# Kernel optimization log

Measured on AMD Instinct MI355X. Metric: run time of the kernel, lower is better.

## Reference

```python
import jax, jax.numpy as jnp
import numpy as np

CTX = 1024   # context_window
D = 512      # emb_dim
B = 8        # batch


def make_rotary_matrix(ctx, d):
    """Dense block-diagonal RoPE rotation matrices R: [ctx, d, d]."""
    pos = jnp.arange(ctx, dtype=jnp.float32)[:, None]          # [ctx, 1]
    i = jnp.arange(d // 2, dtype=jnp.float32)                  # [d/2]
    theta = pos / (10000.0 ** (2.0 * i / d))                   # [ctx, d/2]
    cos, sin = jnp.cos(theta), jnp.sin(theta)
    idx = jnp.arange(d // 2)
    R = jnp.zeros((ctx, d, d), jnp.float32)
    R = R.at[:, 2 * idx, 2 * idx].set(cos)
    R = R.at[:, 2 * idx, 2 * idx + 1].set(-sin)
    R = R.at[:, 2 * idx + 1, 2 * idx].set(sin)
    R = R.at[:, 2 * idx + 1, 2 * idx + 1].set(cos)
    return R


def setup_inputs() -> dict:
    key = jax.random.key(0)
    ks = jax.random.split(key, 8)
    s = 1.0 / np.sqrt(D)
    inp = {
        "x": jax.random.normal(ks[0], (B, CTX, D), jnp.float32),
        "w_q": jax.random.uniform(ks[1], (D, D), jnp.float32, -s, s),
        "b_q": jax.random.uniform(ks[2], (D,), jnp.float32, -s, s),
        "w_k": jax.random.uniform(ks[3], (D, D), jnp.float32, -s, s),
        "b_k": jax.random.uniform(ks[4], (D,), jnp.float32, -s, s),
        "w_v": jax.random.uniform(ks[5], (D, D), jnp.float32, -s, s),
        "b_v": jax.random.uniform(ks[6], (D,), jnp.float32, -s, s),
        "R": make_rotary_matrix(CTX, D),
        "kv_cache": 0,  # bool flag; does not affect output
    }
    return inp


def reference(x, w_q, b_q, w_k, b_k, w_v, b_v, R, kv_cache):
    B_, C, Dm = x.shape
    q = x @ w_q.T + b_q                      # [B, C, D]
    k = x @ w_k.T + b_k
    v = x @ w_v.T + b_v
    Rc = R[:C]                               # [C, D, D]
    # torch.bmm(q.transpose(0,1), R.transpose(1,2)).transpose(0,1)
    # out[b,c,e] = sum_d q[b,c,d] * R[c,e,d]
    q_rot = jnp.einsum("bcd,ced->bce", q, Rc)
    k_rot = jnp.einsum("bcd,ced->bce", k, Rc)
    # causal SDPA (eval mode: dropout omitted)
    scale = 1.0 / jnp.sqrt(jnp.asarray(Dm, jnp.float32))
    scores = jnp.einsum("bqe,bke->bqk", q_rot, k_rot) * scale   # [B, C, C]
    causal = jnp.tril(jnp.ones((C, C), bool))
    scores = jnp.where(causal, scores, jnp.finfo(scores.dtype).min)
    attn = jax.nn.softmax(scores, axis=-1)
    return jnp.einsum("bqk,bkd->bqd", attn, v)
```

## Files before the change

### kernel.cpp

```cpp
#include <hip/hip_runtime.h>

#define BATCH 8
#define CTXN  1024
#define DMODEL 512

using short8  = __attribute__((ext_vector_type(8))) short;
using f32x16  = __attribute__((ext_vector_type(16))) float;

typedef const void __attribute__((address_space(1)))* as1_cvp;
typedef void __attribute__((address_space(3)))* as3_vp;

__device__ __forceinline__ unsigned short f2bf(float f) {
  unsigned int u = __float_as_uint(f);
  u += 0x7fffu + ((u >> 16) & 1u);
  return (unsigned short)(u >> 16);
}
__device__ __forceinline__ float bf2f(unsigned short u) {
  return __uint_as_float((unsigned int)u << 16);
}

#define X4  1048576
#define W4  65536
#define CAST_BLOCKS 4864
__global__ __launch_bounds__(256) void prep_all(const float* __restrict__ x,
                                                const float* __restrict__ wq,
                                                const float* __restrict__ wk,
                                                const float* __restrict__ wv,
                                                unsigned short* __restrict__ xb,
                                                unsigned short* __restrict__ wb,
                                                float2* __restrict__ tab) {
  if (blockIdx.x < CAST_BLOCKS) {
    int gid = blockIdx.x * 256 + threadIdx.x;
    const float4* src; ushort4* dst;
    if (gid < X4)                { src = (const float4*)x  + gid;              dst = (ushort4*)xb + gid; }
    else if (gid < X4 + W4)      { int o = gid - X4;        src = (const float4*)wq + o; dst = (ushort4*)wb + o; }
    else if (gid < X4 + 2 * W4)  { int o = gid - X4 - W4;   src = (const float4*)wk + o; dst = (ushort4*)(wb + 262144) + o; }
    else                         { int o = gid - X4 - 2*W4; src = (const float4*)wv + o; dst = (ushort4*)(wb + 524288) + o; }
    float4 f = *src;
    ushort4 u;
    u.x = f2bf(f.x); u.y = f2bf(f.y); u.z = f2bf(f.z); u.w = f2bf(f.w);
    *dst = u;
  } else {
    int c = blockIdx.x - CAST_BLOCKS;
    int i = threadIdx.x;
    float freq = exp2f((float)i * (-13.287712379549449f / 256.0f));
    float th = (float)c * freq;
    float sn, cs;
    sincosf(th, &sn, &cs);
    tab[c * 256 + i] = make_float2(cs, sn);
  }
}

__device__ __forceinline__ void issue_tile(const unsigned short* __restrict__ gA, int ldA,
                                           const unsigned short* __restrict__ gB, int ldB,
                                           unsigned short* sA, unsigned short* sB,
                                           int slot, int tid) {
  unsigned short* dA = sA + (slot << 13);
  unsigned short* dB = sB + (slot << 13);
#pragma unroll
  for (int c = 0; c < 2; ++c) {
    int li  = (c << 9) + tid;
    int row = li >> 3;
    int ch  = (li & 7) ^ (row & 7);
    __builtin_amdgcn_global_load_lds((as1_cvp)(gA + (size_t)row * ldA + (ch << 3)),
                                     (as3_vp)(dA + (li << 3)), 16, 0, 0);
  }
#pragma unroll
  for (int c = 0; c < 2; ++c) {
    int li  = (c << 9) + tid;
    int row = li >> 3;
    int ch  = (li & 7) ^ (row & 7);
    __builtin_amdgcn_global_load_lds((as1_cvp)(gB + (size_t)row * ldB + (ch << 3)),
                                     (as3_vp)(dB + (li << 3)), 16, 0, 0);
  }
}

__device__ __forceinline__ void gemm_pipe(const unsigned short* __restrict__ gA, int ldA,
                                          const unsigned short* __restrict__ gB, int ldB,
                                          int nt, unsigned short* sA, unsigned short* sB,
                                          int tid, f32x16 acc[2]) {
  const int l = tid & 63, w = tid >> 6, wr = w >> 2, wc = w & 3;
  const int cl = l & 31, hi = l >> 5;
  int aoff[2][4], boff[4];
#pragma unroll
  for (int m = 0; m < 2; ++m) {
    int ra = wr * 64 + m * 32 + cl;
#pragma unroll
    for (int ks = 0; ks < 4; ++ks) {
      int kc = ks * 2 + hi;
      aoff[m][ks] = ra * 64 + ((kc ^ (ra & 7)) << 3);
    }
  }
  {
    int rb = wc * 32 + cl;
#pragma unroll
    for (int ks = 0; ks < 4; ++ks) {
      int kc = ks * 2 + hi;
      boff[ks] = rb * 64 + ((kc ^ (rb & 7)) << 3);
    }
  }
  issue_tile(gA, ldA, gB, ldB, sA, sB, 0, tid);
  issue_tile(gA + 64, ldA, gB + 64, ldB, sA, sB, 1, tid);
  asm volatile("s_waitcnt vmcnt(4)" ::: "memory");
  __builtin_amdgcn_s_barrier();
  __builtin_amdgcn_sched_barrier(0);

  for (int t = 0; t < nt; ++t) {
    const unsigned short* sAb = sA + ((t & 1) << 13);
    const unsigned short* sBb = sB + ((t & 1) << 13);
    short8 af[2][4], bfv[4];
    af[0][0] = *(const short8*)(sAb + aoff[0][0]);
    af[1][0] = *(const short8*)(sAb + aoff[1][0]);
    bfv[0]   = *(const short8*)(sBb + boff[0]);
#pragma unroll
    for (int ks = 0; ks < 3; ++ks) {
      af[0][ks + 1] = *(const short8*)(sAb + aoff[0][ks + 1]);
      af[1][ks + 1] = *(const short8*)(sAb + aoff[1][ks + 1]);
      bfv[ks + 1]   = *(const short8*)(sBb + boff[ks + 1]);
      asm volatile("s_waitcnt lgkmcnt(3)" ::: "memory");
      __builtin_amdgcn_sched_barrier(0);
      __builtin_amdgcn_s_setprio(1);
      acc[0] = __builtin_amdgcn_mfma_f32_32x32x16_bf16(af[0][ks], bfv[ks], acc[0], 0, 0, 0);
      acc[1] = __builtin_amdgcn_mfma_f32_32x32x16_bf16(af[1][ks], bfv[ks], acc[1], 0, 0, 0);
      __builtin_amdgcn_s_setprio(0);
    }
    asm volatile("s_waitcnt lgkmcnt(0)" ::: "memory");
    __builtin_amdgcn_sched_barrier(0);
    __builtin_amdgcn_s_barrier();
    if (t + 2 < nt) {
      issue_tile(gA + (size_t)(t + 2) * 64, ldA, gB + (size_t)(t + 2) * 64, ldB, sA, sB, t & 1, tid);
      asm volatile("s_waitcnt vmcnt(4)" ::: "memory");
    } else {
      asm volatile("s_waitcnt vmcnt(0)" ::: "memory");
    }
    __builtin_amdgcn_sched_barrier(0);
    __builtin_amdgcn_s_setprio(1);
    acc[0] = __builtin_amdgcn_mfma_f32_32x32x16_bf16(af[0][3], bfv[3], acc[0], 0, 0, 0);
    acc[1] = __builtin_amdgcn_mfma_f32_32x32x16_bf16(af[1][3], bfv[3], acc[1], 0, 0, 0);
    __builtin_amdgcn_s_setprio(0);
    __builtin_amdgcn_s_barrier();
    __builtin_amdgcn_sched_barrier(0);
  }
}

__device__ __forceinline__ void issue_tile64(const unsigned short* __restrict__ gA, int ldA,
                                             const unsigned short* __restrict__ gB, int ldB,
                                             unsigned short* sA, unsigned short* sB,
                                             int slot, int tid) {
  unsigned short* dA = sA + (slot << 12);
  unsigned short* dB = sB + (slot << 13);
#pragma unroll
  for (int c = 0; c < 2; ++c) {
    int li  = (c << 8) + tid;
    int row = li >> 3;
    int ch  = (li & 7) ^ (row & 7);
    __builtin_amdgcn_global_load_lds((as1_cvp)(gA + (size_t)row * ldA + (ch << 3)),
                                     (as3_vp)(dA + (li << 3)), 16, 0, 0);
  }
#pragma unroll
  for (int c = 0; c < 4; ++c) {
    int li  = (c << 8) + tid;
    int row = li >> 3;
    int ch  = (li & 7) ^ (row & 7);
    __builtin_amdgcn_global_load_lds((as1_cvp)(gB + (size_t)row * ldB + (ch << 3)),
                                     (as3_vp)(dB + (li << 3)), 16, 0, 0);
  }
}

template <bool RSUM>
__device__ __forceinline__ void gemm_pipe64(const unsigned short* __restrict__ gA, int ldA,
                                            const unsigned short* __restrict__ gB, int ldB,
                                            int nt, unsigned short* sA, unsigned short* sB,
                                            int tid, f32x16 acc[2], float* lacc) {
  const int l = tid & 63, w = tid >> 6;
  const int cl = l & 31, hi = l >> 5;
  int aoff[2][4], boff[4];
#pragma unroll
  for (int m = 0; m < 2; ++m) {
    int ra = m * 32 + cl;
#pragma unroll
    for (int ks = 0; ks < 4; ++ks) {
      int kc = ks * 2 + hi;
      aoff[m][ks] = ra * 64 + ((kc ^ (ra & 7)) << 3);
    }
  }
  {
    int rb = w * 32 + cl;
#pragma unroll
    for (int ks = 0; ks < 4; ++ks) {
      int kc = ks * 2 + hi;
      boff[ks] = rb * 64 + ((kc ^ (rb & 7)) << 3);
    }
  }
  const int srow = tid >> 2;
  const int kc0  = (tid & 3) * 2;
  const int soff0 = srow * 64 + (((kc0)     ^ (srow & 7)) << 3);
  const int soff1 = srow * 64 + (((kc0 + 1) ^ (srow & 7)) << 3);

  issue_tile64(gA, ldA, gB, ldB, sA, sB, 0, tid);
  issue_tile64(gA + 64, ldA, gB + 64, ldB, sA, sB, 1, tid);
  asm volatile("s_waitcnt vmcnt(6)" ::: "memory");
  __builtin_amdgcn_s_barrier();
  __builtin_amdgcn_sched_barrier(0);

  for (int t = 0; t < nt; ++t) {
    const unsigned short* sAb = sA + ((t & 1) << 12);
    const unsigned short* sBb = sB + ((t & 1) << 13);
    short8 af[2][4], bfv[4], sr0, sr1;
    af[0][0] = *(const short8*)(sAb + aoff[0][0]);
    af[1][0] = *(const short8*)(sAb + aoff[1][0]);
    bfv[0]   = *(const short8*)(sBb + boff[0]);
#pragma unroll
    for (int ks = 0; ks < 3; ++ks) {
      af[0][ks + 1] = *(const short8*)(sAb + aoff[0][ks + 1]);
      af[1][ks + 1] = *(const short8*)(sAb + aoff[1][ks + 1]);
      bfv[ks + 1]   = *(const short8*)(sBb + boff[ks + 1]);
      asm volatile("s_waitcnt lgkmcnt(3)" ::: "memory");
      __builtin_amdgcn_sched_barrier(0);
      __builtin_amdgcn_s_setprio(1);
      acc[0] = __builtin_amdgcn_mfma_f32_32x32x16_bf16(af[0][ks], bfv[ks], acc[0], 0, 0, 0);
      acc[1] = __builtin_amdgcn_mfma_f32_32x32x16_bf16(af[1][ks], bfv[ks], acc[1], 0, 0, 0);
      __builtin_amdgcn_s_setprio(0);
    }
    if (RSUM) {
      sr0 = *(const short8*)(sAb + soff0);
      sr1 = *(const short8*)(sAb + soff1);
    }
    asm volatile("s_waitcnt lgkmcnt(0)" ::: "memory");
    __builtin_amdgcn_sched_barrier(0);
    __builtin_amdgcn_s_barrier();
    if (t + 2 < nt) {
      issue_tile64(gA + (size_t)(t + 2) * 64, ldA, gB + (size_t)(t + 2) * 64, ldB, sA, sB, t & 1, tid);
      asm volatile("s_waitcnt vmcnt(6)" ::: "memory");
    } else {
      asm volatile("s_waitcnt vmcnt(0)" ::: "memory");
    }
    __builtin_amdgcn_sched_barrier(0);
    if (RSUM) {
      float ls = 0.0f;
#pragma unroll
      for (int j = 0; j < 8; ++j) ls += bf2f((unsigned short)sr0[j]) + bf2f((unsigned short)sr1[j]);
      *lacc += ls;
    }
    __builtin_amdgcn_s_setprio(1);
    acc[0] = __builtin_amdgcn_mfma_f32_32x32x16_bf16(af[0][3], bfv[3], acc[0], 0, 0, 0);
    acc[1] = __builtin_amdgcn_mfma_f32_32x32x16_bf16(af[1][3], bfv[3], acc[1], 0, 0, 0);
    __builtin_amdgcn_s_setprio(0);
    __builtin_amdgcn_s_barrier();
    __builtin_amdgcn_sched_barrier(0);
  }
}


__global__ __launch_bounds__(512, 4) void qkv_kernel(const unsigned short* __restrict__ xb,
                                                     const unsigned short* __restrict__ wb,
                                                     const float* __restrict__ bq,
                                                     const float* __restrict__ bk,
                                                     const float* __restrict__ bv,
                                                     const float2* __restrict__ tab,
                                                     unsigned short* __restrict__ qrot,
                                                     unsigned short* __restrict__ krot,
                                                     unsigned short* __restrict__ vt) {
  __shared__ __align__(16) unsigned short sA[2 * 8192];
  __shared__ __align__(16) unsigned short sB[2 * 8192];
  int id = blockIdx.x;
  int b3 = id & 7, rest = id >> 3;
  int ntile = rest % 12, mhi = rest / 12;
  int m0 = (mhi * 8 + b3) * 128, n0 = ntile * 128;
  int t = threadIdx.x, w = t >> 6, l = t & 63, wr = w >> 2, wc = w & 3;
  int cl = l & 31, hi = l >> 5;
  f32x16 acc[2] = {};
  gemm_pipe(xb + (size_t)m0 * 512, 512, wb + (size_t)n0 * 512, 512, 8, sA, sB, t, acc);

  int sec = n0 >> 9;
  const float* bias = (sec == 0) ? bq : (sec == 1) ? bk : bv;
  unsigned short* qk_dst = (sec == 0) ? qrot : krot;
  int e = (n0 + wc * 32 + cl) & 511;
  float bsv = bias[e];
  if (sec < 2) {
    int i2 = e >> 1;
#pragma unroll
    for (int m = 0; m < 2; ++m) {
      int rowb = m0 + wr * 64 + m * 32 + 4 * hi;
#pragma unroll
      for (int r = 0; r < 16; ++r) {
        int mg = rowb + (r & 3) + 8 * (r >> 2);
        int cpos = mg & (CTXN - 1);
        float val  = acc[m][r] + bsv;
        float part = __shfl_xor(val, 1);
        float2 cs  = tab[cpos * 256 + i2];
        float o = (e & 1) ? fmaf(part, cs.y, val * cs.x)
                          : fmaf(-part, cs.y, val * cs.x);
        qk_dst[(size_t)mg * 512 + e] = f2bf(o);
      }
    }
  } else {
#pragma unroll
    for (int m = 0; m < 2; ++m) {
      int rowb0 = m0 + wr * 64 + m * 32 + 4 * hi;
#pragma unroll
      for (int q = 0; q < 4; ++q) {
        int rowb = rowb0 + 8 * q;
        int bidx = rowb >> 10;
        int cpos = rowb & (CTXN - 1);
        ushort4 pk;
        pk.x = f2bf(acc[m][q * 4 + 0] + bsv);
        pk.y = f2bf(acc[m][q * 4 + 1] + bsv);
        pk.z = f2bf(acc[m][q * 4 + 2] + bsv);
        pk.w = f2bf(acc[m][q * 4 + 3] + bsv);
        *(ushort4*)(vt + ((size_t)bidx * 512 + e) * 1024 + cpos) = pk;
      }
    }
  }
}

__device__ const unsigned char T64_IT[72] = {
  0,1,2,2,3,3,4,4,4,5,5,5,6,6,6,6,7,7,7,7,
  8,8,8,8,8,9,9,9,9,9,10,10,10,10,10,10,11,11,11,11,11,11,
  12,12,12,12,12,12,12,13,13,13,13,13,13,13,
  14,14,14,14,14,14,14,14,15,15,15,15,15,15,15,15};
__device__ const unsigned char T64_JT[72] = {
  0,0,0,1,0,1,0,1,2,0,1,2,0,1,2,3,0,1,2,3,
  0,1,2,3,4,0,1,2,3,4,0,1,2,3,4,5,0,1,2,3,4,5,
  0,1,2,3,4,5,6,0,1,2,3,4,5,6,
  0,1,2,3,4,5,6,7,0,1,2,3,4,5,6,7};

__global__ __launch_bounds__(256, 3) void scores_kernel(const unsigned short* __restrict__ qr,
                                                        const unsigned short* __restrict__ kr,
                                                        unsigned short* __restrict__ P) {
  int id = blockIdx.x;
  int b = id & 7, tri = id >> 3;
  int it = T64_IT[tri], jt = T64_JT[tri];
  __shared__ __align__(16) unsigned short sA[2 * 4096];
  __shared__ __align__(16) unsigned short sB[2 * 8192];
  int t = threadIdx.x, w = t >> 6, l = t & 63;
  int cl = l & 31, hi = l >> 5;
  const unsigned short* A  = qr + ((size_t)b << 19) + (size_t)it * 64 * 512;
  const unsigned short* Bp = kr + ((size_t)b << 19) + (size_t)jt * 128 * 512;
  f32x16 acc[2] = {};
  float dummy = 0.0f;
  gemm_pipe64<false>(A, 512, Bp, 512, 8, sA, sB, t, acc, &dummy);

  const float scale = 0.04419417382415922f;
  unsigned short* Pb = P + ((size_t)b << 20);
  int j = jt * 128 + w * 32 + cl;
#pragma unroll
  for (int m = 0; m < 2; ++m) {
    int iqb = it * 64 + m * 32 + 4 * hi;
#pragma unroll
    for (int r = 0; r < 16; ++r) {
      int row = iqb + (r & 3) + 8 * (r >> 2);
      float p = (j <= row) ? __expf(acc[m][r] * scale) : 0.0f;
      Pb[(size_t)row * 1024 + j] = f2bf(p);
    }
  }
}

__global__ __launch_bounds__(256, 3) void pv_kernel(const unsigned short* __restrict__ P,
                                                    const unsigned short* __restrict__ vt,
                                                    float* __restrict__ out) {
  int id = blockIdx.x;
  int b = id & 7, rest = id >> 3;
  int pr = rest & 7, nt2 = rest >> 3;
  __shared__ __align__(16) unsigned short sA[2 * 4096];
  __shared__ __align__(16) unsigned short sB[2 * 8192];
  __shared__ float lpart[64][4];
  __shared__ float lsum[64];
  int t = threadIdx.x, w = t >> 6, l = t & 63;
  int cl = l & 31, hi = l >> 5;
  const unsigned short* Bp = vt + ((size_t)b << 19) + (size_t)nt2 * 128 * 1024;
  float* ob = out + ((size_t)b << 19);
  int d = nt2 * 128 + w * 32 + cl;

#pragma unroll
  for (int h = 0; h < 2; ++h) {
    int it = h ? (15 - pr) : pr;
    const unsigned short* A = P + ((size_t)b << 20) + (size_t)it * 64 * 1024;
    int nt = ((it >> 1) + 1) * 2;
    f32x16 acc[2] = {};
    float lacc = 0.0f;
    gemm_pipe64<true>(A, 1024, Bp, 1024, nt, sA, sB, t, acc, &lacc);

    lpart[t >> 2][t & 3] = lacc;
    __syncthreads();
    if (t < 64) lsum[t] = (lpart[t][0] + lpart[t][1]) + (lpart[t][2] + lpart[t][3]);
    __syncthreads();

#pragma unroll
    for (int m = 0; m < 2; ++m) {
      int rl0 = m * 32 + 4 * hi;
#pragma unroll
      for (int r = 0; r < 16; ++r) {
        int rl = rl0 + (r & 3) + 8 * (r >> 2);
        ob[(size_t)(it * 64 + rl) * 512 + d] = acc[m][r] * (1.0f / lsum[rl]);
      }
    }
    __syncthreads();
  }
}

extern "C" void kernel_launch(void* const* d_in, const int* in_sizes, int n_in,
                              void* d_out, int out_size, void* d_ws, size_t ws_size,
                              hipStream_t stream) {
  const float* x  = (const float*)d_in[0];
  const float* wq = (const float*)d_in[1];
  const float* bq = (const float*)d_in[2];
  const float* wk = (const float*)d_in[3];
  const float* bk = (const float*)d_in[4];
  const float* wv = (const float*)d_in[5];
  const float* bv = (const float*)d_in[6];
  float* out = (float*)d_out;

  char* ws = (char*)d_ws;
  float2*         tab  = (float2*)(ws);
  unsigned short* xb   = (unsigned short*)(ws + (2ull  << 20));
  unsigned short* wb   = (unsigned short*)(ws + (10ull << 20));
  unsigned short* qrot = (unsigned short*)(ws + (12ull << 20));
  unsigned short* krot = (unsigned short*)(ws + (20ull << 20));
  unsigned short* vt   = (unsigned short*)(ws + (28ull << 20));
  unsigned short* P    = (unsigned short*)(ws + (36ull << 20));

  prep_all<<<dim3(CAST_BLOCKS + CTXN), dim3(256), 0, stream>>>(x, wq, wk, wv, xb, wb, tab);
  qkv_kernel<<<dim3(768), dim3(512), 0, stream>>>(xb, wb, bq, bk, bv, tab, qrot, krot, vt);
  scores_kernel<<<dim3(576), dim3(256), 0, stream>>>(qrot, krot, P);
  pv_kernel<<<dim3(256), dim3(256), 0, stream>>>(P, vt, out);
}
```

Baseline: 65.40 us.

## Fuse x fp32-to-bf16 cast into QKV GEMM A-tile loading

Removes the separate pass that converts x to bf16 in the prep kernel. The QKV GEMM now loads fp32 x rows into registers, converts them to bf16, and writes them into swizzled LDS, double-buffered against the B tiles. This avoids writing and re-reading a 16MB bf16 copy of x. In exchange each QKV block reads twice as many A bytes and does the conversion inline, with register staging in place of async global-to-LDS loads, and x is re-read by all 12 N-tiles.

```diff
diff --git a/kernel.cpp b/kernel.cpp
--- a/kernel.cpp
+++ b/kernel.cpp
@@ -19,29 +19,25 @@
   return __uint_as_float((unsigned int)u << 16);
 }
 
-#define X4  1048576
 #define W4  65536
-#define CAST_BLOCKS 4864
-__global__ __launch_bounds__(256) void prep_all(const float* __restrict__ x,
-                                                const float* __restrict__ wq,
+#define WCAST_BLOCKS 768
+__global__ __launch_bounds__(256) void prep_all(const float* __restrict__ wq,
                                                 const float* __restrict__ wk,
                                                 const float* __restrict__ wv,
-                                                unsigned short* __restrict__ xb,
                                                 unsigned short* __restrict__ wb,
                                                 float2* __restrict__ tab) {
-  if (blockIdx.x < CAST_BLOCKS) {
+  if (blockIdx.x < WCAST_BLOCKS) {
     int gid = blockIdx.x * 256 + threadIdx.x;
     const float4* src; ushort4* dst;
-    if (gid < X4)                { src = (const float4*)x  + gid;              dst = (ushort4*)xb + gid; }
-    else if (gid < X4 + W4)      { int o = gid - X4;        src = (const float4*)wq + o; dst = (ushort4*)wb + o; }
-    else if (gid < X4 + 2 * W4)  { int o = gid - X4 - W4;   src = (const float4*)wk + o; dst = (ushort4*)(wb + 262144) + o; }
-    else                         { int o = gid - X4 - 2*W4; src = (const float4*)wv + o; dst = (ushort4*)(wb + 524288) + o; }
+    if (gid < W4)            { src = (const float4*)wq + gid;            dst = (ushort4*)wb + gid; }
+    else if (gid < 2 * W4)   { int o = gid - W4;     src = (const float4*)wk + o; dst = (ushort4*)(wb + 262144) + o; }
+    else                     { int o = gid - 2 * W4; src = (const float4*)wv + o; dst = (ushort4*)(wb + 524288) + o; }
     float4 f = *src;
     ushort4 u;
     u.x = f2bf(f.x); u.y = f2bf(f.y); u.z = f2bf(f.z); u.w = f2bf(f.w);
     *dst = u;
   } else {
-    int c = blockIdx.x - CAST_BLOCKS;
+    int c = blockIdx.x - WCAST_BLOCKS;
     int i = threadIdx.x;
     float freq = exp2f((float)i * (-13.287712379549449f / 256.0f));
     float th = (float)c * freq;
@@ -51,20 +47,33 @@
   }
 }
 
-__device__ __forceinline__ void issue_tile(const unsigned short* __restrict__ gA, int ldA,
-                                           const unsigned short* __restrict__ gB, int ldB,
-                                           unsigned short* sA, unsigned short* sB,
-                                           int slot, int tid) {
-  unsigned short* dA = sA + (slot << 13);
-  unsigned short* dB = sB + (slot << 13);
+__device__ __forceinline__ void loadA_f32(const float* __restrict__ g, float4 aR[4], int tid) {
 #pragma unroll
   for (int c = 0; c < 2; ++c) {
     int li  = (c << 9) + tid;
     int row = li >> 3;
-    int ch  = (li & 7) ^ (row & 7);
-    __builtin_amdgcn_global_load_lds((as1_cvp)(gA + (size_t)row * ldA + (ch << 3)),
-                                     (as3_vp)(dA + (li << 3)), 16, 0, 0);
-  }
+    int chs = (li & 7) ^ (row & 7);
+    const float4* p = (const float4*)(g + (size_t)row * 512 + (chs << 3));
+    aR[c * 2 + 0] = p[0];
+    aR[c * 2 + 1] = p[1];
+  }
+}
+__device__ __forceinline__ void writeA(unsigned short* sA, int slot, const float4 aR[4], int tid) {
+#pragma unroll
+  for (int c = 0; c < 2; ++c) {
+    int li = (c << 9) + tid;
+    const float4 f0 = aR[c * 2 + 0], f1 = aR[c * 2 + 1];
+    short8 v;
+    v[0] = (short)f2bf(f0.x); v[1] = (short)f2bf(f0.y);
+    v[2] = (short)f2bf(f0.z); v[3] = (short)f2bf(f0.w);
+    v[4] = (short)f2bf(f1.x); v[5] = (short)f2bf(f1.y);
+    v[6] = (short)f2bf(f1.z); v[7] = (short)f2bf(f1.w);
+    *(short8*)(sA + (slot << 13) + (li << 3)) = v;
+  }
+}
+__device__ __forceinline__ void issueB(const unsigned short* __restrict__ gB, int ldB,
+                                       unsigned short* sB, int slot, int tid) {
+  unsigned short* dB = sB + (slot << 13);
 #pragma unroll
   for (int c = 0; c < 2; ++c) {
     int li  = (c << 9) + tid;
@@ -75,10 +84,10 @@
   }
 }
 
-__device__ __forceinline__ void gemm_pipe(const unsigned short* __restrict__ gA, int ldA,
-                                          const unsigned short* __restrict__ gB, int ldB,
-                                          int nt, unsigned short* sA, unsigned short* sB,
-                                          int tid, f32x16 acc[2]) {
+__device__ __forceinline__ void gemm_pipe_xf32(const float* __restrict__ gA,
+                                               const unsigned short* __restrict__ gB, int ldB,
+                                               unsigned short* sA, unsigned short* sB,
+                                               int tid, f32x16 acc[2]) {
   const int l = tid & 63, w = tid >> 6, wr = w >> 2, wc = w & 3;
   const int cl = l & 31, hi = l >> 5;
   int aoff[2][4], boff[4];
@@ -99,13 +108,19 @@
       boff[ks] = rb * 64 + ((kc ^ (rb & 7)) << 3);
     }
   }
-  issue_tile(gA, ldA, gB, ldB, sA, sB, 0, tid);
-  issue_tile(gA + 64, ldA, gB + 64, ldB, sA, sB, 1, tid);
-  asm volatile("s_waitcnt vmcnt(4)" ::: "memory");
+  float4 aR0[4], aR1[4];
+  loadA_f32(gA, aR0, tid);
+  issueB(gB, ldB, sB, 0, tid);
+  loadA_f32(gA + 64, aR1, tid);
+  issueB(gB + 64, ldB, sB, 1, tid);
+  asm volatile("s_waitcnt vmcnt(6)" ::: "memory");
+  writeA(sA, 0, aR0, tid);
+  asm volatile("s_waitcnt lgkmcnt(0)" ::: "memory");
   __builtin_amdgcn_s_barrier();
   __builtin_amdgcn_sched_barrier(0);
 
-  for (int t = 0; t < nt; ++t) {
+#pragma unroll
+  for (int t = 0; t < 8; ++t) {
     const unsigned short* sAb = sA + ((t & 1) << 13);
     const unsigned short* sBb = sB + ((t & 1) << 13);
     short8 af[2][4], bfv[4];
@@ -127,17 +142,25 @@
     asm volatile("s_waitcnt lgkmcnt(0)" ::: "memory");
     __builtin_amdgcn_sched_barrier(0);
     __builtin_amdgcn_s_barrier();
-    if (t + 2 < nt) {
-      issue_tile(gA + (size_t)(t + 2) * 64, ldA, gB + (size_t)(t + 2) * 64, ldB, sA, sB, t & 1, tid);
-      asm volatile("s_waitcnt vmcnt(4)" ::: "memory");
+    if (t + 2 < 8) {
+      if (t & 1) loadA_f32(gA + (size_t)(t + 2) * 64, aR1, tid);
+      else       loadA_f32(gA + (size_t)(t + 2) * 64, aR0, tid);
+      issueB(gB + (size_t)(t + 2) * 64, ldB, sB, t & 1, tid);
+      asm volatile("s_waitcnt vmcnt(6)" ::: "memory");
     } else {
       asm volatile("s_waitcnt vmcnt(0)" ::: "memory");
     }
     __builtin_amdgcn_sched_barrier(0);
+    if (t + 1 < 8) {
+      if (t & 1) writeA(sA, (t + 1) & 1, aR0, tid);
+      else       writeA(sA, (t + 1) & 1, aR1, tid);
+    }
     __builtin_amdgcn_s_setprio(1);
     acc[0] = __builtin_amdgcn_mfma_f32_32x32x16_bf16(af[0][3], bfv[3], acc[0], 0, 0, 0);
     acc[1] = __builtin_amdgcn_mfma_f32_32x32x16_bf16(af[1][3], bfv[3], acc[1], 0, 0, 0);
     __builtin_amdgcn_s_setprio(0);
+    asm volatile("s_waitcnt lgkmcnt(0)" ::: "memory");
+    __builtin_amdgcn_sched_barrier(0);
     __builtin_amdgcn_s_barrier();
     __builtin_amdgcn_sched_barrier(0);
   }
@@ -252,7 +275,7 @@
 }
 
 
-__global__ __launch_bounds__(512, 4) void qkv_kernel(const unsigned short* __restrict__ xb,
+__global__ __launch_bounds__(512, 4) void qkv_kernel(const float* __restrict__ x,
                                                      const unsigned short* __restrict__ wb,
                                                      const float* __restrict__ bq,
                                                      const float* __restrict__ bk,
@@ -270,7 +293,7 @@
   int t = threadIdx.x, w = t >> 6, l = t & 63, wr = w >> 2, wc = w & 3;
   int cl = l & 31, hi = l >> 5;
   f32x16 acc[2] = {};
-  gemm_pipe(xb + (size_t)m0 * 512, 512, wb + (size_t)n0 * 512, 512, 8, sA, sB, t, acc);
+  gemm_pipe_xf32(x + (size_t)m0 * 512, wb + (size_t)n0 * 512, 512, sA, sB, t, acc);
 
   int sec = n0 >> 9;
   const float* bias = (sec == 0) ? bq : (sec == 1) ? bk : bv;
@@ -413,15 +436,14 @@
 
   char* ws = (char*)d_ws;
   float2*         tab  = (float2*)(ws);
-  unsigned short* xb   = (unsigned short*)(ws + (2ull  << 20));
   unsigned short* wb   = (unsigned short*)(ws + (10ull << 20));
   unsigned short* qrot = (unsigned short*)(ws + (12ull << 20));
   unsigned short* krot = (unsigned short*)(ws + (20ull << 20));
   unsigned short* vt   = (unsigned short*)(ws + (28ull << 20));
   unsigned short* P    = (unsigned short*)(ws + (36ull << 20));
 
-  prep_all<<<dim3(CAST_BLOCKS + CTXN), dim3(256), 0, stream>>>(x, wq, wk, wv, xb, wb, tab);
-  qkv_kernel<<<dim3(768), dim3(512), 0, stream>>>(xb, wb, bq, bk, bv, tab, qrot, krot, vt);
+  prep_all<<<dim3(WCAST_BLOCKS + CTXN), dim3(256), 0, stream>>>(wq, wk, wv, wb, tab);
+  qkv_kernel<<<dim3(768), dim3(512), 0, stream>>>(x, wb, bq, bk, bv, tab, qrot, krot, vt);
   scores_kernel<<<dim3(576), dim3(256), 0, stream>>>(qrot, krot, P);
   pv_kernel<<<dim3(256), dim3(256), 0, stream>>>(P, vt, out);
 }
```

Result: slower. 71.29 us (median of 2 runs) (+9.0%).
